# Optimization experiments

Hardware: AMD Instinct MI355X
Metric: run time of the kernel (lower is better)

## Reference

```python
import jax, jax.numpy as jnp
import numpy as np

N, E, IN = 100000, 1600000, 128
H, C = 4, 16            # heads, out_channels
HID = H * C             # concat output dim = 64
SLOPE = 0.2             # GATv2Conv negative_slope default
EPS = 1e-5              # LayerNorm eps


def setup_inputs() -> dict:
    key = jax.random.key(0)
    ks = jax.random.split(key, 12)
    s = 0.05
    x = jax.random.normal(ks[0], (N, IN), jnp.float32)
    edge_index = jax.random.randint(ks[1], (2, E), 0, N, dtype=jnp.int32)
    return {
        "x": x,
        "edge_index": edge_index,
        # GATv2Conv params (lin_l: source, lin_r: target; both with bias)
        "W_l": jax.random.normal(ks[2], (IN, HID), jnp.float32) * s,
        "b_l": jnp.zeros((HID,), jnp.float32),
        "W_r": jax.random.normal(ks[3], (IN, HID), jnp.float32) * s,
        "b_r": jnp.zeros((HID,), jnp.float32),
        "att": jax.random.normal(ks[4], (H, C), jnp.float32) * s,
        "bias": jnp.zeros((HID,), jnp.float32),
        # residual projection Linear(in, heads*out, bias=False)
        "W_res": jax.random.normal(ks[5], (IN, HID), jnp.float32) * s,
        # pyg LayerNorm affine params
        "ln_w": jnp.ones((HID,), jnp.float32),
        "ln_b": jnp.zeros((HID,), jnp.float32),
    }


def reference(x, edge_index, W_l, b_l, W_r, b_r, att, bias, W_res, ln_w, ln_b):
    n = x.shape[0]
    # GATv2Conv adds self-loops by default
    loops = jnp.arange(n, dtype=edge_index.dtype)
    src = jnp.concatenate([edge_index[0], loops])  # message source j
    dst = jnp.concatenate([edge_index[1], loops])  # message target i

    xl = (x @ W_l + b_l).reshape(n, H, C)  # source-side projection
    xr = (x @ W_r + b_r).reshape(n, H, C)  # target-side projection

    # GATv2 attention: e_ij = att . LeakyReLU(xl_j + xr_i)
    e = jax.nn.leaky_relu(xl[src] + xr[dst], SLOPE)   # [Et, H, C]
    score = jnp.einsum('ehc,hc->eh', e, att)          # [Et, H]

    # segment softmax over incoming edges of each target node
    smax = jax.ops.segment_max(score, dst, num_segments=n)
    ex = jnp.exp(score - smax[dst])
    ssum = jax.ops.segment_sum(ex, dst, num_segments=n)
    alpha = ex / (ssum[dst] + 1e-16)                  # [Et, H]

    # weighted scatter-add of source features, concat heads
    msg = xl[src] * alpha[..., None]                  # [Et, H, C]
    out = jax.ops.segment_sum(msg, dst, num_segments=n).reshape(n, HID)
    out = out + bias + x @ W_res                      # bias + residual

    # pyg.nn.LayerNorm(mode='graph', batch=None): global mean/std over all elems
    out = out - out.mean()
    out = out / (out.std() + EPS)
    return out * ln_w + ln_b
```

## Files before the change

### kernel.cpp

```cpp
#include <hip/hip_runtime.h>
#include <math.h>

#define SLOPE  0.2f
#define LN_EPS 1e-5f
#define HID    64
#define IN_DIM 128
#define BM     64
#define KH     64

__global__ __launch_bounds__(256) void proj_kernel(
    const float* __restrict__ x,
    const float* __restrict__ Wl, const float* __restrict__ bl,
    const float* __restrict__ Wr, const float* __restrict__ br,
    const float* __restrict__ Wres,
    float* __restrict__ xl, float* __restrict__ xr, float* __restrict__ out_un,
    int n)
{
    __shared__ float xs[BM][KH + 4];
    int t    = threadIdx.x;
    int mat  = blockIdx.x % 3;
    int tile = blockIdx.x / 3;
    int row0 = tile * BM;

    const float* __restrict__ W = (mat == 0) ? Wl : (mat == 1) ? Wr : Wres;
    float* __restrict__       O = (mat == 0) ? xl : (mat == 1) ? xr : out_un;

    int cb = (t & 15) * 4;
    int ry = (t >> 4) * 4;

    float4 binit = make_float4(0.f, 0.f, 0.f, 0.f);
    if (mat == 0)      binit = *(const float4*)&bl[cb];
    else if (mat == 1) binit = *(const float4*)&br[cb];

    float4 acc[4];
#pragma unroll
    for (int r = 0; r < 4; ++r) acc[r] = binit;

    for (int h = 0; h < 2; ++h) {
#pragma unroll
        for (int p = 0; p < 4; ++p) {
            int f  = t + p * 256;
            int r  = f >> 4;
            int c4 = f & 15;
            float4 v = make_float4(0.f, 0.f, 0.f, 0.f);
            if (row0 + r < n)
                v = ((const float4*)x)[(long)(row0 + r) * 32 + h * 16 + c4];
            *(float4*)&xs[r][c4 * 4] = v;
        }
        __syncthreads();

        for (int k4 = 0; k4 < 16; ++k4) {
            float4 xv[4];
#pragma unroll
            for (int r = 0; r < 4; ++r)
                xv[r] = *(const float4*)&xs[ry + r][k4 * 4];
#pragma unroll
            for (int kk = 0; kk < 4; ++kk) {
                int k = h * KH + k4 * 4 + kk;
                float4 w = *(const float4*)&W[k * HID + cb];
#pragma unroll
                for (int r = 0; r < 4; ++r) {
                    float xvk = (kk == 0) ? xv[r].x : (kk == 1) ? xv[r].y
                              : (kk == 2) ? xv[r].z : xv[r].w;
                    acc[r].x = fmaf(xvk, w.x, acc[r].x);
                    acc[r].y = fmaf(xvk, w.y, acc[r].y);
                    acc[r].z = fmaf(xvk, w.z, acc[r].z);
                    acc[r].w = fmaf(xvk, w.w, acc[r].w);
                }
            }
        }
        __syncthreads();
    }

#pragma unroll
    for (int r = 0; r < 4; ++r) {
        long ro = row0 + ry + r;
        if (ro < n) *(float4*)&O[ro * HID + cb] = acc[r];
    }
}

__global__ void deg_zero_kernel(int* __restrict__ deg, int n) {
    for (int i = blockIdx.x * blockDim.x + threadIdx.x; i < n; i += gridDim.x * blockDim.x)
        deg[i] = 0;
}

__global__ __launch_bounds__(256) void rank_kernel(
    const int* __restrict__ dst, int* __restrict__ deg, int* __restrict__ rank, int e)
{
    int tid = blockIdx.x * blockDim.x + threadIdx.x;
    int stride = gridDim.x * blockDim.x;
    int e4 = e >> 2;
    for (int i = tid; i < e4; i += stride) {
        int4 d = ((const int4*)dst)[i];
        int r0 = atomicAdd(&deg[d.x], 1);
        int r1 = atomicAdd(&deg[d.y], 1);
        int r2 = atomicAdd(&deg[d.z], 1);
        int r3 = atomicAdd(&deg[d.w], 1);
        ((int4*)rank)[i] = make_int4(r0, r1, r2, r3);
    }
    for (int i = (e4 << 2) + tid; i < e; i += stride)
        rank[i] = atomicAdd(&deg[dst[i]], 1);
}

__global__ __launch_bounds__(1024) void scan_kernel(
    const int* __restrict__ deg, int* __restrict__ off, int* __restrict__ csr, int n)
{
    __shared__ int wsum[16];
    __shared__ int carry_s;
    int t = threadIdx.x, lane = t & 63, w = t >> 6;
    if (t == 0) carry_s = 0;
    __syncthreads();
    for (int base = 0; base < n; base += 4096) {
        int i0 = base + t * 4;
        int4 v = make_int4(0, 0, 0, 0);
        if (i0 + 3 < n) {
            int4 dv = *(const int4*)&deg[i0];
            v = make_int4(dv.x + 1, dv.y + 1, dv.z + 1, dv.w + 1);
        } else if (i0 < n) {
            v.x = deg[i0] + 1;
            if (i0 + 1 < n) v.y = deg[i0 + 1] + 1;
            if (i0 + 2 < n) v.z = deg[i0 + 2] + 1;
        }
        int local = v.x + v.y + v.z + v.w;
        int inc = local;
#pragma unroll
        for (int d = 1; d < 64; d <<= 1) {
            int o = __shfl_up(inc, d, 64);
            if (lane >= d) inc += o;
        }
        if (lane == 63) wsum[w] = inc;
        __syncthreads();
        if (w == 0 && lane < 16) {
            int s = wsum[lane];
#pragma unroll
            for (int d = 1; d < 16; d <<= 1) {
                int o = __shfl_up(s, d, 16);
                if (lane >= d) s += o;
            }
            wsum[lane] = s;
        }
        __syncthreads();
        int woff = (w > 0) ? wsum[w - 1] : 0;
        int bc = carry_s;
        __syncthreads();
        int o0 = bc + woff + inc - local;
        int o1 = o0 + v.x, o2 = o1 + v.y, o3 = o2 + v.z, o4 = o3 + v.w;
        if (i0     < n) { off[i0]     = o0; csr[o1 - 1] = i0;     }
        if (i0 + 1 < n) { off[i0 + 1] = o1; csr[o2 - 1] = i0 + 1; }
        if (i0 + 2 < n) { off[i0 + 2] = o2; csr[o3 - 1] = i0 + 2; }
        if (i0 + 3 < n) { off[i0 + 3] = o3; csr[o4 - 1] = i0 + 3; }
        if (t == 1023) carry_s = bc + wsum[15];
        __syncthreads();
    }
    if (threadIdx.x == 0) off[n] = carry_s;
}

__global__ __launch_bounds__(256) void place_kernel(
    const int* __restrict__ src, const int* __restrict__ dst,
    const int* __restrict__ rank, const int* __restrict__ off,
    int* __restrict__ csr, int e)
{
    int tid = blockIdx.x * blockDim.x + threadIdx.x;
    int stride = gridDim.x * blockDim.x;
    int e4 = e >> 2;
    for (int i = tid; i < e4; i += stride) {
        int4 d = ((const int4*)dst)[i];
        int4 s = ((const int4*)src)[i];
        int4 r = ((const int4*)rank)[i];
        int o0 = off[d.x], o1 = off[d.y], o2 = off[d.z], o3 = off[d.w];
        csr[o0 + r.x] = s.x;
        csr[o1 + r.y] = s.y;
        csr[o2 + r.z] = s.z;
        csr[o3 + r.w] = s.w;
    }
    for (int i = (e4 << 2) + tid; i < e; i += stride)
        csr[off[dst[i]] + rank[i]] = src[i];
}

__global__ __launch_bounds__(256) void attn_kernel(
    const float* __restrict__ xl, const float* __restrict__ xr,
    const float* __restrict__ att, const float* __restrict__ bias,
    const int* __restrict__ off, const int* __restrict__ csr,
    float* __restrict__ out_un,
    float2* __restrict__ partials, int n)
{
    const int l    = threadIdx.x & 63;
    const int wid  = threadIdx.x >> 6;
    const int g    = l >> 4;
    const int r    = l & 15;
    const int node = blockIdx.x * 4 + wid;

    float s1 = 0.0f, s2 = 0.0f;
    if (node < n) {
        const float4 a4  = ((const float4*)att)[r];
        const float4 xr4 = ((const float4*)xr)[node * 16 + r];

        int e0 = off[node], e1 = off[node + 1];
        int nit = (e1 - e0 + 3) >> 2;

        float m = -1e30f, ssum = 0.0f;
        float4 acc = make_float4(0.f, 0.f, 0.f, 0.f);

        for (int it = 0; it < nit; ++it) {
            int eidx = e0 + it * 4 + g;
            bool valid = eidx < e1;
            int j = csr[valid ? eidx : e1 - 1];
            float4 v = ((const float4*)xl)[j * 16 + r];
            float tx = v.x + xr4.x, ty = v.y + xr4.y;
            float tz = v.z + xr4.z, tw = v.w + xr4.w;
            tx = fmaxf(tx, SLOPE * tx); ty = fmaxf(ty, SLOPE * ty);
            tz = fmaxf(tz, SLOPE * tz); tw = fmaxf(tw, SLOPE * tw);
            float p = fmaf(tw, a4.w, fmaf(tz, a4.z, fmaf(ty, a4.y, tx * a4.x)));
            p += __shfl_xor(p, 1);
            p += __shfl_xor(p, 2);
            float s  = valid ? p : -INFINITY;
            float nm = fmaxf(m, s);
            float eo = __expf(m - nm);
            float pe = __expf(s - nm);
            acc.x = acc.x * eo + pe * v.x;
            acc.y = acc.y * eo + pe * v.y;
            acc.z = acc.z * eo + pe * v.z;
            acc.w = acc.w * eo + pe * v.w;
            ssum  = ssum * eo + pe;
            m = nm;
        }

#pragma unroll
        for (int mask = 16; mask <= 32; mask <<= 1) {
            float om = __shfl_xor(m, mask);
            float os = __shfl_xor(ssum, mask);
            float ox = __shfl_xor(acc.x, mask);
            float oy = __shfl_xor(acc.y, mask);
            float oz = __shfl_xor(acc.z, mask);
            float ow = __shfl_xor(acc.w, mask);
            float nm = fmaxf(m, om);
            float f1 = __expf(m - nm);
            float f2 = __expf(om - nm);
            acc.x = acc.x * f1 + ox * f2;
            acc.y = acc.y * f1 + oy * f2;
            acc.z = acc.z * f1 + oz * f2;
            acc.w = acc.w * f1 + ow * f2;
            ssum  = ssum * f1 + os * f2;
            m = nm;
        }

        float inv = 1.0f / (ssum + 1e-16f);
        if (l < 16) {
            float4 b4  = ((const float4*)bias)[r];
            float4 res = ((const float4*)out_un)[node * 16 + r];
            float4 ro;
            ro.x = acc.x * inv + b4.x + res.x;
            ro.y = acc.y * inv + b4.y + res.y;
            ro.z = acc.z * inv + b4.z + res.z;
            ro.w = acc.w * inv + b4.w + res.w;
            ((float4*)out_un)[node * 16 + r] = ro;
            s1 = ro.x + ro.y + ro.z + ro.w;
            s2 = ro.x * ro.x + ro.y * ro.y + ro.z * ro.z + ro.w * ro.w;
        }
    }

#pragma unroll
    for (int d = 32; d; d >>= 1) {
        s1 += __shfl_xor(s1, d, 64);
        s2 += __shfl_xor(s2, d, 64);
    }
    __shared__ float bs[8];
    if (l == 0) { bs[wid] = s1; bs[4 + wid] = s2; }
    __syncthreads();
    if (threadIdx.x == 0)
        partials[blockIdx.x] = make_float2(bs[0] + bs[1] + bs[2] + bs[3],
                                           bs[4] + bs[5] + bs[6] + bs[7]);
}

__global__ __launch_bounds__(1024) void reduce_kernel(
    const float2* __restrict__ partials, double* __restrict__ red, int nb)
{
    double a = 0.0, b = 0.0;
    for (int i = threadIdx.x; i < nb; i += 1024) {
        float2 p = partials[i];
        a += (double)p.x; b += (double)p.y;
    }
#pragma unroll
    for (int d = 32; d; d >>= 1) {
        a += __shfl_xor(a, d, 64);
        b += __shfl_xor(b, d, 64);
    }
    __shared__ double sa[16], sb[16];
    int w = threadIdx.x >> 6;
    if ((threadIdx.x & 63) == 0) { sa[w] = a; sb[w] = b; }
    __syncthreads();
    if (threadIdx.x == 0) {
        double ta = 0.0, tb = 0.0;
#pragma unroll
        for (int k = 0; k < 16; ++k) { ta += sa[k]; tb += sb[k]; }
        red[0] = ta; red[1] = tb;
    }
}

__global__ void ln_kernel(const float* __restrict__ out_un, const double* __restrict__ red,
                          const float* __restrict__ ln_w, const float* __restrict__ ln_b,
                          float* __restrict__ out, int total )
{
    double cnt  = (double)total;
    double mu   = red[0] / cnt;
    double var  = red[1] / cnt - mu * mu;
    float mean  = (float)mu;
    float inv   = 1.0f / (sqrtf((float)(var > 0.0 ? var : 0.0)) + LN_EPS);
    int n4 = total >> 2;
    for (int i = blockIdx.x * blockDim.x + threadIdx.x; i < n4; i += gridDim.x * blockDim.x) {
        float4 v = ((const float4*)out_un)[i];
        int cb = (i << 2) & 63;
        float4 r;
        r.x = (v.x - mean) * inv * ln_w[cb + 0] + ln_b[cb + 0];
        r.y = (v.y - mean) * inv * ln_w[cb + 1] + ln_b[cb + 1];
        r.z = (v.z - mean) * inv * ln_w[cb + 2] + ln_b[cb + 2];
        r.w = (v.w - mean) * inv * ln_w[cb + 3] + ln_b[cb + 3];
        ((float4*)out)[i] = r;
    }
}

extern "C" void kernel_launch(void* const* d_in, const int* in_sizes, int n_in,
                              void* d_out, int out_size, void* d_ws, size_t ws_size,
                              hipStream_t stream)
{
    const float* x    = (const float*)d_in[0];
    const int*   ei   = (const int*)d_in[1];
    const float* Wl   = (const float*)d_in[2];
    const float* bl   = (const float*)d_in[3];
    const float* Wr   = (const float*)d_in[4];
    const float* br   = (const float*)d_in[5];
    const float* att  = (const float*)d_in[6];
    const float* bias = (const float*)d_in[7];
    const float* Wres = (const float*)d_in[8];
    const float* lnw  = (const float*)d_in[9];
    const float* lnb  = (const float*)d_in[10];

    int n = in_sizes[0] / IN_DIM;
    int e = in_sizes[1] / 2;
    const int* src = ei;
    const int* dst = ei + e;

    int nblocks = (n + 3) / 4;
    int ntiles  = (n + BM - 1) / BM;

    char* w = (char*)d_ws;
    double* red    = (double*)w;
    float* xl      = (float*)(w + 256);
    float* xr      = xl + (long)n * HID;
    float* out_un  = xr + (long)n * HID;
    int*   deg     = (int*)(out_un + (long)n * HID);
    int*   off     = deg + n;
    int*   csr     = off + n + 1;
    int*    rank     = (int*)out_un;
    float2* partials = (float2*)deg;

    deg_zero_kernel<<<512, 256, 0, stream>>>(deg, n);
    rank_kernel<<<2048, 256, 0, stream>>>(dst, deg, rank, e);
    scan_kernel<<<1, 1024, 0, stream>>>(deg, off, csr, n);
    place_kernel<<<2048, 256, 0, stream>>>(src, dst, rank, off, csr, e);

    proj_kernel<<<3 * ntiles, 256, 0, stream>>>(x, Wl, bl, Wr, br, Wres,
                                                xl, xr, out_un, n);

    attn_kernel<<<nblocks, 256, 0, stream>>>(xl, xr, att, bias, off, csr,
                                             out_un, partials, n);
    reduce_kernel<<<1, 1024, 0, stream>>>(partials, red, nblocks);

    ln_kernel<<<4096, 256, 0, stream>>>(out_un, red, lnw, lnb, (float*)d_out, n * HID);
}
```

Baseline: 478.5 us.

## Fuse CSR placement and projection GEMM into one interleaved launch

Merges the edge placement kernel and the three-matrix projection kernel into a single launch where every fourth block does CSR placement and the rest compute projection tiles. The goal is to overlap memory-bound scatter work with the compute-bound GEMM and save a launch. The rank buffer moves to the output buffer so it no longer aliases out_un, and the degree zeroing now uses hipMemsetAsync. The risk is that placement blocks with one grid-stride loop get uneven work, and that the shared-memory footprint stays allocated for placement blocks.

```diff
diff --git a/kernel.cpp b/kernel.cpp
--- a/kernel.cpp
+++ b/kernel.cpp
@@ -7,82 +7,6 @@
 #define IN_DIM 128
 #define BM     64
 #define KH     64
-
-__global__ __launch_bounds__(256) void proj_kernel(
-    const float* __restrict__ x,
-    const float* __restrict__ Wl, const float* __restrict__ bl,
-    const float* __restrict__ Wr, const float* __restrict__ br,
-    const float* __restrict__ Wres,
-    float* __restrict__ xl, float* __restrict__ xr, float* __restrict__ out_un,
-    int n)
-{
-    __shared__ float xs[BM][KH + 4];
-    int t    = threadIdx.x;
-    int mat  = blockIdx.x % 3;
-    int tile = blockIdx.x / 3;
-    int row0 = tile * BM;
-
-    const float* __restrict__ W = (mat == 0) ? Wl : (mat == 1) ? Wr : Wres;
-    float* __restrict__       O = (mat == 0) ? xl : (mat == 1) ? xr : out_un;
-
-    int cb = (t & 15) * 4;
-    int ry = (t >> 4) * 4;
-
-    float4 binit = make_float4(0.f, 0.f, 0.f, 0.f);
-    if (mat == 0)      binit = *(const float4*)&bl[cb];
-    else if (mat == 1) binit = *(const float4*)&br[cb];
-
-    float4 acc[4];
-#pragma unroll
-    for (int r = 0; r < 4; ++r) acc[r] = binit;
-
-    for (int h = 0; h < 2; ++h) {
-#pragma unroll
-        for (int p = 0; p < 4; ++p) {
-            int f  = t + p * 256;
-            int r  = f >> 4;
-            int c4 = f & 15;
-            float4 v = make_float4(0.f, 0.f, 0.f, 0.f);
-            if (row0 + r < n)
-                v = ((const float4*)x)[(long)(row0 + r) * 32 + h * 16 + c4];
-            *(float4*)&xs[r][c4 * 4] = v;
-        }
-        __syncthreads();
-
-        for (int k4 = 0; k4 < 16; ++k4) {
-            float4 xv[4];
-#pragma unroll
-            for (int r = 0; r < 4; ++r)
-                xv[r] = *(const float4*)&xs[ry + r][k4 * 4];
-#pragma unroll
-            for (int kk = 0; kk < 4; ++kk) {
-                int k = h * KH + k4 * 4 + kk;
-                float4 w = *(const float4*)&W[k * HID + cb];
-#pragma unroll
-                for (int r = 0; r < 4; ++r) {
-                    float xvk = (kk == 0) ? xv[r].x : (kk == 1) ? xv[r].y
-                              : (kk == 2) ? xv[r].z : xv[r].w;
-                    acc[r].x = fmaf(xvk, w.x, acc[r].x);
-                    acc[r].y = fmaf(xvk, w.y, acc[r].y);
-                    acc[r].z = fmaf(xvk, w.z, acc[r].z);
-                    acc[r].w = fmaf(xvk, w.w, acc[r].w);
-                }
-            }
-        }
-        __syncthreads();
-    }
-
-#pragma unroll
-    for (int r = 0; r < 4; ++r) {
-        long ro = row0 + ry + r;
-        if (ro < n) *(float4*)&O[ro * HID + cb] = acc[r];
-    }
-}
-
-__global__ void deg_zero_kernel(int* __restrict__ deg, int n) {
-    for (int i = blockIdx.x * blockDim.x + threadIdx.x; i < n; i += gridDim.x * blockDim.x)
-        deg[i] = 0;
-}
 
 __global__ __launch_bounds__(256) void rank_kernel(
     const int* __restrict__ dst, int* __restrict__ deg, int* __restrict__ rank, int e)
@@ -155,26 +79,99 @@
     if (threadIdx.x == 0) off[n] = carry_s;
 }
 
-__global__ __launch_bounds__(256) void place_kernel(
+__global__ __launch_bounds__(256) void fused_pp_kernel(
     const int* __restrict__ src, const int* __restrict__ dst,
     const int* __restrict__ rank, const int* __restrict__ off,
-    int* __restrict__ csr, int e)
-{
-    int tid = blockIdx.x * blockDim.x + threadIdx.x;
-    int stride = gridDim.x * blockDim.x;
-    int e4 = e >> 2;
-    for (int i = tid; i < e4; i += stride) {
-        int4 d = ((const int4*)dst)[i];
-        int4 s = ((const int4*)src)[i];
-        int4 r = ((const int4*)rank)[i];
-        int o0 = off[d.x], o1 = off[d.y], o2 = off[d.z], o3 = off[d.w];
-        csr[o0 + r.x] = s.x;
-        csr[o1 + r.y] = s.y;
-        csr[o2 + r.z] = s.z;
-        csr[o3 + r.w] = s.w;
-    }
-    for (int i = (e4 << 2) + tid; i < e; i += stride)
-        csr[off[dst[i]] + rank[i]] = src[i];
+    int* __restrict__ csr, int e, int nPlaceBlocks,
+    const float* __restrict__ x,
+    const float* __restrict__ Wl, const float* __restrict__ bl,
+    const float* __restrict__ Wr, const float* __restrict__ br,
+    const float* __restrict__ Wres,
+    float* __restrict__ xl, float* __restrict__ xr, float* __restrict__ out_un,
+    int n)
+{
+    __shared__ float xs[BM][KH + 4];
+    int t    = threadIdx.x;
+    int grp  = blockIdx.x >> 2;
+    int sub  = blockIdx.x & 3;
+
+    if (sub == 0) {
+        int tid = grp * 256 + t;
+        int stride = nPlaceBlocks * 256;
+        int e4 = e >> 2;
+        for (int i = tid; i < e4; i += stride) {
+            int4 d = ((const int4*)dst)[i];
+            int4 s = ((const int4*)src)[i];
+            int4 r = ((const int4*)rank)[i];
+            int o0 = off[d.x], o1 = off[d.y], o2 = off[d.z], o3 = off[d.w];
+            csr[o0 + r.x] = s.x;
+            csr[o1 + r.y] = s.y;
+            csr[o2 + r.z] = s.z;
+            csr[o3 + r.w] = s.w;
+        }
+        for (int i = (e4 << 2) + tid; i < e; i += stride)
+            csr[off[dst[i]] + rank[i]] = src[i];
+        return;
+    }
+
+    int mat  = sub - 1;
+    int row0 = grp * BM;
+
+    const float* __restrict__ W = (mat == 0) ? Wl : (mat == 1) ? Wr : Wres;
+    float* __restrict__       O = (mat == 0) ? xl : (mat == 1) ? xr : out_un;
+
+    int cb = (t & 15) * 4;
+    int ry = (t >> 4) * 4;
+
+    float4 binit = make_float4(0.f, 0.f, 0.f, 0.f);
+    if (mat == 0)      binit = *(const float4*)&bl[cb];
+    else if (mat == 1) binit = *(const float4*)&br[cb];
+
+    float4 acc[4];
+#pragma unroll
+    for (int r = 0; r < 4; ++r) acc[r] = binit;
+
+    for (int h = 0; h < 2; ++h) {
+#pragma unroll
+        for (int p = 0; p < 4; ++p) {
+            int f  = t + p * 256;
+            int r  = f >> 4;
+            int c4 = f & 15;
+            float4 v = make_float4(0.f, 0.f, 0.f, 0.f);
+            if (row0 + r < n)
+                v = ((const float4*)x)[(long)(row0 + r) * 32 + h * 16 + c4];
+            *(float4*)&xs[r][c4 * 4] = v;
+        }
+        __syncthreads();
+
+        for (int k4 = 0; k4 < 16; ++k4) {
+            float4 xv[4];
+#pragma unroll
+            for (int r = 0; r < 4; ++r)
+                xv[r] = *(const float4*)&xs[ry + r][k4 * 4];
+#pragma unroll
+            for (int kk = 0; kk < 4; ++kk) {
+                int k = h * KH + k4 * 4 + kk;
+                float4 w = *(const float4*)&W[k * HID + cb];
+#pragma unroll
+                for (int r = 0; r < 4; ++r) {
+                    float xvk = (kk == 0) ? xv[r].x : (kk == 1) ? xv[r].y
+                              : (kk == 2) ? xv[r].z : xv[r].w;
+                    acc[r].x = fmaf(xvk, w.x, acc[r].x);
+                    acc[r].y = fmaf(xvk, w.y, acc[r].y);
+                    acc[r].z = fmaf(xvk, w.z, acc[r].z);
+                    acc[r].w = fmaf(xvk, w.w, acc[r].w);
+                }
+            }
+        }
+        __syncthreads();
+    }
+
+#pragma unroll
+    for (int r = 0; r < 4; ++r) {
+        long ro = row0 + ry + r;
+        if (ro < n) *(float4*)&O[ro * HID + cb] = acc[r];
+    }
 }
 
 __global__ __launch_bounds__(256) void attn_kernel(
@@ -351,16 +348,16 @@
     int*   deg     = (int*)(out_un + (long)n * HID);
     int*   off     = deg + n;
     int*   csr     = off + n + 1;
-    int*    rank     = (int*)out_un;
+    int*    rank     = (int*)d_out;
     float2* partials = (float2*)deg;
 
-    deg_zero_kernel<<<512, 256, 0, stream>>>(deg, n);
+    hipMemsetAsync(deg, 0, n * sizeof(int), stream);
     rank_kernel<<<2048, 256, 0, stream>>>(dst, deg, rank, e);
     scan_kernel<<<1, 1024, 0, stream>>>(deg, off, csr, n);
-    place_kernel<<<2048, 256, 0, stream>>>(src, dst, rank, off, csr, e);
-
-    proj_kernel<<<3 * ntiles, 256, 0, stream>>>(x, Wl, bl, Wr, br, Wres,
-                                                xl, xr, out_un, n);
+
+    fused_pp_kernel<<<4 * ntiles, 256, 0, stream>>>(
+        src, dst, rank, off, csr, e, ntiles,
+        x, Wl, bl, Wr, br, Wres, xl, xr, out_un, n);
 
     attn_kernel<<<nblocks, 256, 0, stream>>>(xl, xr, att, bias, off, csr,
                                              out_un, partials, n);
```

After: 499.9 us. 4.5% more time.
